# Kernel tuning notes

Hardware: AMD Instinct MI355X
Metric: run time of the kernel (lower is better)

## Reference

```python
import jax, jax.numpy as jnp
import numpy as np

NUM_EMBEDDINGS = 1024
EMBEDDING_DIM = 64
COMMIT_COST = 0.25


def setup_inputs() -> dict:
    key = jax.random.key(0)
    k1, k2 = jax.random.split(key)
    latent = jax.random.normal(k1, (32, EMBEDDING_DIM, 32, 32), dtype=jnp.float32)
    embedding_weight = jax.random.normal(k2, (NUM_EMBEDDINGS, EMBEDDING_DIM), dtype=jnp.float32)
    return {"latent": latent, "embedding_weight": embedding_weight}


def reference(latent, embedding_weight):
    # rearrange 'b n j d -> b j d n'; n == embedding_dim
    lat = jnp.transpose(latent, (0, 2, 3, 1))  # [b, j, d, n]
    flat = lat.reshape(-1, EMBEDDING_DIM)      # [T, D]
    # squared-euclidean distances [T, K]
    distances = (
        jnp.sum(flat ** 2, axis=1, keepdims=True)
        + jnp.sum(embedding_weight ** 2, axis=1)
        - 2.0 * flat @ embedding_weight.T
    )
    idx = jnp.argmin(distances, axis=1)                         # [T]
    encodings = jax.nn.one_hot(idx, NUM_EMBEDDINGS, dtype=flat.dtype)  # [T, K]
    quantized_flat = embedding_weight[idx]                      # gather == encodings @ W
    quantized = quantized_flat.reshape(lat.shape)               # [b, j, d, n]

    e_latent_loss = jnp.mean((jax.lax.stop_gradient(quantized) - lat) ** 2)
    loss = COMMIT_COST * e_latent_loss

    # straight-through estimator
    quantized_st = lat + jax.lax.stop_gradient(quantized - lat)

    avg_probs = jnp.mean(encodings, axis=0)
    perplexity = jnp.exp(-jnp.sum(avg_probs * jnp.log(avg_probs + 1e-10)))

    # rearrange back 'b j d n -> b n j d'
    quantized_out = jnp.transpose(quantized_st, (0, 3, 1, 2))
    return quantized_out, loss, perplexity, encodings, distances
```

## Files before the change

### kernel.cpp

```cpp
#include <hip/hip_runtime.h>
#include <cfloat>

#define T_TOTAL 32768
#define DIM 64
#define KCODES 1024

static constexpr long long OFF_Q    = 0;
static constexpr long long OFF_LOSS = 2097152;
static constexpr long long OFF_PERP = 2097153;
static constexpr long long OFF_ENC  = 2097154;
static constexpr long long OFF_DIST = 2097154LL + 33554432LL;


__global__ __launch_bounds__(256) void vq_ww_kernel(const float* __restrict__ W,
                                                    float* __restrict__ ww) {
    const int tid  = threadIdx.x;
    const int lane = tid & 63;
    const int code = blockIdx.x * 4 + (tid >> 6);
    float v = W[code * DIM + lane];
    float s = v * v;
    #pragma unroll
    for (int off = 32; off > 0; off >>= 1)
        s += __shfl_down(s, off, 64);
    if (lane == 0) ww[code] = s;
}

__global__ __launch_bounds__(256) void vq_main_kernel(const float* __restrict__ lat,
                                                      const float* __restrict__ W,
                                                      const float* __restrict__ ww,
                                                      float* __restrict__ out,
                                                      int* __restrict__ counts,
                                                      float* __restrict__ lossSum) {
    __shared__ float xT[64 * 64];
    __shared__ float wS[64 * 65];
    __shared__ float xx[64];
    __shared__ float redV[64 * 16];
    __shared__ int   redI[64 * 16];
    __shared__ int   selIdx[64];

    const int tid = threadIdx.x;
    const int tx  = tid & 15;
    const int ty  = tid >> 4;
    const int t0  = blockIdx.x * 64;
    const long long base = (long long)(t0 >> 10) * 65536 + (long long)(t0 & 1023);

    #pragma unroll
    for (int i = 0; i < 16; ++i) {
        int e  = i * 256 + tid;
        int n  = e >> 6;
        int tl = e & 63;
        xT[n * 64 + tl] = lat[base + (long long)n * 1024 + tl];
    }
    __syncthreads();
    if (tid < 64) {
        float s = 0.f;
        #pragma unroll 8
        for (int n = 0; n < 64; ++n) {
            float v = xT[n * 64 + tid];
            s = fmaf(v, v, s);
        }
        xx[tid] = s;
    }

    float minV[4] = {FLT_MAX, FLT_MAX, FLT_MAX, FLT_MAX};
    int   minI[4] = {0, 0, 0, 0};

    float* __restrict__ distOut = out + OFF_DIST;

    for (int c = 0; c < 16; ++c) {
        __syncthreads();
        {
            const float4* __restrict__ Wv = (const float4*)(W + c * 4096);
            #pragma unroll
            for (int i = 0; i < 4; ++i) {
                int e2 = i * 256 + tid;
                float4 v = Wv[e2];
                int kl = e2 >> 4;
                int n0 = (e2 & 15) * 4;
                float* p = &wS[kl * 65 + n0];
                p[0] = v.x; p[1] = v.y; p[2] = v.z; p[3] = v.w;
            }
        }
        __syncthreads();

        float acc[4][4] = {{0.f,0.f,0.f,0.f},{0.f,0.f,0.f,0.f},{0.f,0.f,0.f,0.f},{0.f,0.f,0.f,0.f}};
        #pragma unroll 8
        for (int n = 0; n < 64; ++n) {
            float4 a = *(const float4*)&xT[n * 64 + ty * 4];
            float b0 = wS[(tx * 4 + 0) * 65 + n];
            float b1 = wS[(tx * 4 + 1) * 65 + n];
            float b2 = wS[(tx * 4 + 2) * 65 + n];
            float b3 = wS[(tx * 4 + 3) * 65 + n];
            acc[0][0] = fmaf(a.x, b0, acc[0][0]);
            acc[0][1] = fmaf(a.x, b1, acc[0][1]);
            acc[0][2] = fmaf(a.x, b2, acc[0][2]);
            acc[0][3] = fmaf(a.x, b3, acc[0][3]);
            acc[1][0] = fmaf(a.y, b0, acc[1][0]);
            acc[1][1] = fmaf(a.y, b1, acc[1][1]);
            acc[1][2] = fmaf(a.y, b2, acc[1][2]);
            acc[1][3] = fmaf(a.y, b3, acc[1][3]);
            acc[2][0] = fmaf(a.z, b0, acc[2][0]);
            acc[2][1] = fmaf(a.z, b1, acc[2][1]);
            acc[2][2] = fmaf(a.z, b2, acc[2][2]);
            acc[2][3] = fmaf(a.z, b3, acc[2][3]);
            acc[3][0] = fmaf(a.w, b0, acc[3][0]);
            acc[3][1] = fmaf(a.w, b1, acc[3][1]);
            acc[3][2] = fmaf(a.w, b2, acc[3][2]);
            acc[3][3] = fmaf(a.w, b3, acc[3][3]);
        }

        const int kbase = c * 64 + tx * 4;
        float w0 = ww[kbase + 0];
        float w1 = ww[kbase + 1];
        float w2 = ww[kbase + 2];
        float w3 = ww[kbase + 3];
        #pragma unroll
        for (int qr = 0; qr < 4; ++qr) {
            const int row = ty * 4 + qr;
            const float xxr = xx[row];
            float d0 = (xxr + w0) - 2.f * acc[qr][0];
            float d1 = (xxr + w1) - 2.f * acc[qr][1];
            float d2 = (xxr + w2) - 2.f * acc[qr][2];
            float d3 = (xxr + w3) - 2.f * acc[qr][3];
            if (d0 < minV[qr]) { minV[qr] = d0; minI[qr] = kbase + 0; }
            if (d1 < minV[qr]) { minV[qr] = d1; minI[qr] = kbase + 1; }
            if (d2 < minV[qr]) { minV[qr] = d2; minI[qr] = kbase + 2; }
            if (d3 < minV[qr]) { minV[qr] = d3; minI[qr] = kbase + 3; }
            const long long ro = (long long)(t0 + row) * KCODES + kbase;
            *(float2*)&distOut[ro]     = make_float2(d0, d1);
            *(float2*)&distOut[ro + 2] = make_float2(d2, d3);
        }
    }

    #pragma unroll
    for (int qr = 0; qr < 4; ++qr) {
        const int row = ty * 4 + qr;
        redV[row * 16 + tx] = minV[qr];
        redI[row * 16 + tx] = minI[qr];
    }
    __syncthreads();
    if (tid < 64) {
        float best = redV[tid * 16];
        int   bi   = redI[tid * 16];
        #pragma unroll
        for (int s = 1; s < 16; ++s) {
            float v  = redV[tid * 16 + s];
            int   i2 = redI[tid * 16 + s];
            if (v < best || (v == best && i2 < bi)) { best = v; bi = i2; }
        }
        selIdx[tid] = bi;
        atomicAdd(&counts[bi], 1);
    }
    __syncthreads();

    float* qS = wS;
    #pragma unroll
    for (int i = 0; i < 16; ++i) {
        int e   = i * 256 + tid;
        int row = e >> 6;
        int n   = e & 63;
        qS[row * 65 + n] = W[selIdx[row] * DIM + n];
    }
    __syncthreads();

    float ls = 0.f;
    #pragma unroll
    for (int i = 0; i < 4; ++i) {
        int e2  = i * 256 + tid;
        int n   = e2 >> 4;
        int tl0 = (e2 & 15) * 4;
        float q0 = qS[(tl0 + 0) * 65 + n];
        float q1 = qS[(tl0 + 1) * 65 + n];
        float q2 = qS[(tl0 + 2) * 65 + n];
        float q3 = qS[(tl0 + 3) * 65 + n];
        float x0 = xT[n * 64 + tl0 + 0];
        float x1 = xT[n * 64 + tl0 + 1];
        float x2 = xT[n * 64 + tl0 + 2];
        float x3 = xT[n * 64 + tl0 + 3];
        *(float4*)&out[OFF_Q + base + (long long)n * 1024 + tl0] = make_float4(q0, q1, q2, q3);
        float e0 = q0 - x0; ls = fmaf(e0, e0, ls);
        float e1 = q1 - x1; ls = fmaf(e1, e1, ls);
        float e2d = q2 - x2; ls = fmaf(e2d, e2d, ls);
        float e3 = q3 - x3; ls = fmaf(e3, e3, ls);
    }
    #pragma unroll
    for (int off = 32; off > 0; off >>= 1)
        ls += __shfl_down(ls, off, 64);
    if ((tid & 63) == 0) atomicAdd(lossSum, ls);

    float* __restrict__ enc = out + OFF_ENC;
    for (int i = 0; i < 128; ++i) {
        int e2  = i * 256 + tid;
        int row = e2 >> 9;
        int k2  = (e2 & 511) * 2;
        int sel = selIdx[row];
        float2 v;
        v.x = (k2     == sel) ? 1.f : 0.f;
        v.y = (k2 + 1 == sel) ? 1.f : 0.f;
        *(float2*)&enc[(long long)(t0 + row) * KCODES + k2] = v;
    }
}

__global__ __launch_bounds__(1024) void vq_finalize_kernel(const int* __restrict__ counts,
                                                           const float* __restrict__ lossSum,
                                                           float* __restrict__ out) {
    __shared__ float red[16];
    const int tid = threadIdx.x;
    float p = (float)counts[tid] * (1.0f / 32768.0f);
    float term = p * logf(p + 1e-10f);
    #pragma unroll
    for (int off = 32; off > 0; off >>= 1)
        term += __shfl_down(term, off, 64);
    if ((tid & 63) == 0) red[tid >> 6] = term;
    __syncthreads();
    if (tid == 0) {
        float s = 0.f;
        #pragma unroll
        for (int i = 0; i < 16; ++i) s += red[i];
        out[OFF_PERP] = expf(-s);
        out[OFF_LOSS] = 0.25f * lossSum[0] * (1.0f / 2097152.0f);
    }
}

extern "C" void kernel_launch(void* const* d_in, const int* in_sizes, int n_in,
                              void* d_out, int out_size, void* d_ws, size_t ws_size,
                              hipStream_t stream) {
    (void)in_sizes; (void)n_in; (void)out_size; (void)ws_size;
    const float* lat = (const float*)d_in[0];
    const float* W   = (const float*)d_in[1];
    float* out = (float*)d_out;

    int*   counts  = (int*)d_ws;
    float* ww      = (float*)((char*)d_ws + 4096);
    float* lossSum = (float*)((char*)d_ws + 8192);

    hipMemsetAsync(d_ws, 0, 8192 + 16, stream);

    vq_ww_kernel<<<256, 256, 0, stream>>>(W, ww);
    vq_main_kernel<<<512, 256, 0, stream>>>(lat, W, ww, out, counts, lossSum);
    vq_finalize_kernel<<<1, 1024, 0, stream>>>(counts, lossSum, out);
}
```

Before: 356.8 us.

## Enlarge per-thread register tile to 8x8 and pre-transpose codebook

```diff
diff --git a/kernel.cpp b/kernel.cpp
--- a/kernel.cpp
+++ b/kernel.cpp
@@ -12,35 +12,44 @@
 static constexpr long long OFF_DIST = 2097154LL + 33554432LL;
 
 
-__global__ __launch_bounds__(256) void vq_ww_kernel(const float* __restrict__ W,
-                                                    float* __restrict__ ww) {
-    const int tid  = threadIdx.x;
-    const int lane = tid & 63;
-    const int code = blockIdx.x * 4 + (tid >> 6);
-    float v = W[code * DIM + lane];
-    float s = v * v;
-    #pragma unroll
-    for (int off = 32; off > 0; off >>= 1)
-        s += __shfl_down(s, off, 64);
-    if (lane == 0) ww[code] = s;
-}
-
-__global__ __launch_bounds__(256) void vq_main_kernel(const float* __restrict__ lat,
-                                                      const float* __restrict__ W,
-                                                      const float* __restrict__ ww,
-                                                      float* __restrict__ out,
-                                                      int* __restrict__ counts,
-                                                      float* __restrict__ lossSum) {
+__global__ __launch_bounds__(256) void vq_prep_kernel(const float* __restrict__ W,
+                                                      float* __restrict__ ww,
+                                                      float* __restrict__ WT) {
+    const int tid = threadIdx.x;
+    if (blockIdx.x < 256) {
+        const int lane = tid & 63;
+        const int code = blockIdx.x * 4 + (tid >> 6);
+        float v = W[code * DIM + lane];
+        float s = v * v;
+        #pragma unroll
+        for (int off = 32; off > 0; off >>= 1)
+            s += __shfl_down(s, off, 64);
+        if (lane == 0) ww[code] = s;
+    } else {
+        const int n = blockIdx.x - 256;
+        #pragma unroll
+        for (int i = 0; i < 4; ++i) {
+            int k = i * 256 + tid;
+            WT[n * KCODES + k] = W[k * DIM + n];
+        }
+    }
+}
+
+__global__ __launch_bounds__(256, 3) void vq_main_kernel(const float* __restrict__ lat,
+                                                         const float* __restrict__ W,
+                                                         const float* __restrict__ ww,
+                                                         const float* __restrict__ WT,
+                                                         float* __restrict__ out,
+                                                         int* __restrict__ counts,
+                                                         float* __restrict__ lossSum) {
     __shared__ float xT[64 * 64];
-    __shared__ float wS[64 * 65];
+    __shared__ float wS[32 * 256];
     __shared__ float xx[64];
-    __shared__ float redV[64 * 16];
-    __shared__ int   redI[64 * 16];
     __shared__ int   selIdx[64];
 
     const int tid = threadIdx.x;
-    const int tx  = tid & 15;
-    const int ty  = tid >> 4;
+    const int tx  = tid & 31;
+    const int ty  = tid >> 5;
     const int t0  = blockIdx.x * 64;
     const long long base = (long long)(t0 >> 10) * 65536 + (long long)(t0 & 1023);
 
@@ -62,90 +71,91 @@
         xx[tid] = s;
     }
 
-    float minV[4] = {FLT_MAX, FLT_MAX, FLT_MAX, FLT_MAX};
-    int   minI[4] = {0, 0, 0, 0};
+    float minV[8];
+    int   minI[8];
+    #pragma unroll
+    for (int r = 0; r < 8; ++r) { minV[r] = FLT_MAX; minI[r] = 0; }
 
     float* __restrict__ distOut = out + OFF_DIST;
 
-    for (int c = 0; c < 16; ++c) {
-        __syncthreads();
-        {
-            const float4* __restrict__ Wv = (const float4*)(W + c * 4096);
+    for (int c = 0; c < 4; ++c) {
+        float acc[8][8];
+        #pragma unroll
+        for (int r = 0; r < 8; ++r)
             #pragma unroll
-            for (int i = 0; i < 4; ++i) {
+            for (int k = 0; k < 8; ++k) acc[r][k] = 0.f;
+
+        for (int h = 0; h < 2; ++h) {
+            __syncthreads();
+            #pragma unroll
+            for (int i = 0; i < 8; ++i) {
                 int e2 = i * 256 + tid;
-                float4 v = Wv[e2];
-                int kl = e2 >> 4;
-                int n0 = (e2 & 15) * 4;
-                float* p = &wS[kl * 65 + n0];
-                p[0] = v.x; p[1] = v.y; p[2] = v.z; p[3] = v.w;
+                int n  = e2 >> 6;
+                int k4 = e2 & 63;
+                *(float4*)&wS[n * 256 + k4 * 4] =
+                    *(const float4*)&WT[(h * 32 + n) * KCODES + c * 256 + k4 * 4];
             }
-        }
-        __syncthreads();
-
-        float acc[4][4] = {{0.f,0.f,0.f,0.f},{0.f,0.f,0.f,0.f},{0.f,0.f,0.f,0.f},{0.f,0.f,0.f,0.f}};
-        #pragma unroll 8
-        for (int n = 0; n < 64; ++n) {
-            float4 a = *(const float4*)&xT[n * 64 + ty * 4];
-            float b0 = wS[(tx * 4 + 0) * 65 + n];
-            float b1 = wS[(tx * 4 + 1) * 65 + n];
-            float b2 = wS[(tx * 4 + 2) * 65 + n];
-            float b3 = wS[(tx * 4 + 3) * 65 + n];
-            acc[0][0] = fmaf(a.x, b0, acc[0][0]);
-            acc[0][1] = fmaf(a.x, b1, acc[0][1]);
-            acc[0][2] = fmaf(a.x, b2, acc[0][2]);
-            acc[0][3] = fmaf(a.x, b3, acc[0][3]);
-            acc[1][0] = fmaf(a.y, b0, acc[1][0]);
-            acc[1][1] = fmaf(a.y, b1, acc[1][1]);
-            acc[1][2] = fmaf(a.y, b2, acc[1][2]);
-            acc[1][3] = fmaf(a.y, b3, acc[1][3]);
-            acc[2][0] = fmaf(a.z, b0, acc[2][0]);
-            acc[2][1] = fmaf(a.z, b1, acc[2][1]);
-            acc[2][2] = fmaf(a.z, b2, acc[2][2]);
-            acc[2][3] = fmaf(a.z, b3, acc[2][3]);
-            acc[3][0] = fmaf(a.w, b0, acc[3][0]);
-            acc[3][1] = fmaf(a.w, b1, acc[3][1]);
-            acc[3][2] = fmaf(a.w, b2, acc[3][2]);
-            acc[3][3] = fmaf(a.w, b3, acc[3][3]);
-        }
-
-        const int kbase = c * 64 + tx * 4;
-        float w0 = ww[kbase + 0];
-        float w1 = ww[kbase + 1];
-        float w2 = ww[kbase + 2];
-        float w3 = ww[kbase + 3];
-        #pragma unroll
-        for (int qr = 0; qr < 4; ++qr) {
-            const int row = ty * 4 + qr;
+            __syncthreads();
+
+            #pragma unroll 4
+            for (int nn = 0; nn < 32; ++nn) {
+                const float* xrow = &xT[(h * 32 + nn) * 64];
+                const float* wrow = &wS[nn * 256];
+                float4 a0 = *(const float4*)&xrow[ty * 4];
+                float4 a1 = *(const float4*)&xrow[32 + ty * 4];
+                float4 b0 = *(const float4*)&wrow[tx * 4];
+                float4 b1 = *(const float4*)&wrow[128 + tx * 4];
+                float ar[8] = {a0.x, a0.y, a0.z, a0.w, a1.x, a1.y, a1.z, a1.w};
+                float br[8] = {b0.x, b0.y, b0.z, b0.w, b1.x, b1.y, b1.z, b1.w};
+                #pragma unroll
+                for (int r = 0; r < 8; ++r)
+                    #pragma unroll
+                    for (int k = 0; k < 8; ++k)
+                        acc[r][k] = fmaf(ar[r], br[k], acc[r][k]);
+            }
+        }
+
+        const int kb0 = c * 256 + tx * 4;
+        float wr[8];
+        #pragma unroll
+        for (int k = 0; k < 8; ++k)
+            wr[k] = ww[kb0 + (k >> 2) * 128 + (k & 3)];
+        #pragma unroll
+        for (int r = 0; r < 8; ++r) {
+            const int row = (r >> 2) * 32 + ty * 4 + (r & 3);
             const float xxr = xx[row];
-            float d0 = (xxr + w0) - 2.f * acc[qr][0];
-            float d1 = (xxr + w1) - 2.f * acc[qr][1];
-            float d2 = (xxr + w2) - 2.f * acc[qr][2];
-            float d3 = (xxr + w3) - 2.f * acc[qr][3];
-            if (d0 < minV[qr]) { minV[qr] = d0; minI[qr] = kbase + 0; }
-            if (d1 < minV[qr]) { minV[qr] = d1; minI[qr] = kbase + 1; }
-            if (d2 < minV[qr]) { minV[qr] = d2; minI[qr] = kbase + 2; }
-            if (d3 < minV[qr]) { minV[qr] = d3; minI[qr] = kbase + 3; }
-            const long long ro = (long long)(t0 + row) * KCODES + kbase;
-            *(float2*)&distOut[ro]     = make_float2(d0, d1);
-            *(float2*)&distOut[ro + 2] = make_float2(d2, d3);
-        }
-    }
-
-    #pragma unroll
-    for (int qr = 0; qr < 4; ++qr) {
-        const int row = ty * 4 + qr;
-        redV[row * 16 + tx] = minV[qr];
-        redI[row * 16 + tx] = minI[qr];
+            float d[8];
+            #pragma unroll
+            for (int k = 0; k < 8; ++k) {
+                d[k] = (xxr + wr[k]) - 2.f * acc[r][k];
+                int ki = kb0 + (k >> 2) * 128 + (k & 3);
+                if (d[k] < minV[r]) { minV[r] = d[k]; minI[r] = ki; }
+            }
+            const long long ro = (long long)(t0 + row) * KCODES + kb0;
+            *(float2*)&distOut[ro]           = make_float2(d[0], d[1]);
+            *(float2*)&distOut[ro + 2]       = make_float2(d[2], d[3]);
+            *(float2*)&distOut[ro + 128]     = make_float2(d[4], d[5]);
+            *(float2*)&distOut[ro + 130]     = make_float2(d[6], d[7]);
+        }
+    }
+
+    __syncthreads();
+    float* redV = wS;
+    int*   redI = (int*)(wS + 64 * 33);
+    #pragma unroll
+    for (int r = 0; r < 8; ++r) {
+        const int row = (r >> 2) * 32 + ty * 4 + (r & 3);
+        redV[row * 33 + tx] = minV[r];
+        redI[row * 33 + tx] = minI[r];
     }
     __syncthreads();
     if (tid < 64) {
-        float best = redV[tid * 16];
-        int   bi   = redI[tid * 16];
-        #pragma unroll
-        for (int s = 1; s < 16; ++s) {
-            float v  = redV[tid * 16 + s];
-            int   i2 = redI[tid * 16 + s];
+        float best = redV[tid * 33];
+        int   bi   = redI[tid * 33];
+        #pragma unroll
+        for (int s = 1; s < 32; ++s) {
+            float v  = redV[tid * 33 + s];
+            int   i2 = redI[tid * 33 + s];
             if (v < best || (v == best && i2 < bi)) { best = v; bi = i2; }
         }
         selIdx[tid] = bi;
@@ -233,10 +243,11 @@
     int*   counts  = (int*)d_ws;
     float* ww      = (float*)((char*)d_ws + 4096);
     float* lossSum = (float*)((char*)d_ws + 8192);
+    float* WT      = (float*)((char*)d_ws + 12288);
 
     hipMemsetAsync(d_ws, 0, 8192 + 16, stream);
 
-    vq_ww_kernel<<<256, 256, 0, stream>>>(W, ww);
-    vq_main_kernel<<<512, 256, 0, stream>>>(lat, W, ww, out, counts, lossSum);
+    vq_prep_kernel<<<320, 256, 0, stream>>>(W, ww, WT);
+    vq_main_kernel<<<512, 256, 0, stream>>>(lat, W, ww, WT, out, counts, lossSum);
     vq_finalize_kernel<<<1, 1024, 0, stream>>>(counts, lossSum, out);
 }
```

After: 340.2 us. 1.05x faster.
